# Kernel tuning notes

Hardware: AMD Instinct MI355X
Metric: run time of the kernel (lower is better)

Reference implementation:

```python
import jax, jax.numpy as jnp
import numpy as np

B, P, N, E = 32, 1024, 1024, 128
HQ = 128  # head_num * qkv_dim == embedding_dim
SQRT_E = 11.313708498984761
LOGIT_CLIP = 10.0


def setup_inputs() -> dict:
    key = jax.random.key(0)
    ks = jax.random.split(key, 16)
    s = 1.0 / np.sqrt(E)
    return {
        "encoded_nodes": jax.random.normal(ks[0], (B, N, E), jnp.float32),
        "encoded_q1": jax.random.normal(ks[1], (B, P, E), jnp.float32),
        "encoded_q2": jax.random.normal(ks[2], (B, P, E), jnp.float32),
        "encoded_last_node": jax.random.normal(ks[3], (B, P, E), jnp.float32),
        "load": jax.random.uniform(ks[4], (B, P), jnp.float32),
        "left": jax.random.uniform(ks[5], (B, P), jnp.float32),
        "cur_dist": jax.random.uniform(ks[6], (B, P, N), jnp.float32),
        "log_scale": jnp.ones((), jnp.float32),
        "ninf_mask": jnp.zeros((B, P, N), jnp.float32),
        "Wq1": jax.random.normal(ks[7], (E, HQ), jnp.float32) * s,
        "Wq2": jax.random.normal(ks[8], (E, HQ), jnp.float32) * s,
        "Wq_last": jax.random.normal(ks[9], (E + 2, HQ), jnp.float32) * s,
        "Wk": jax.random.normal(ks[10], (E, HQ), jnp.float32) * s,
        "Wv": jax.random.normal(ks[11], (E, HQ), jnp.float32) * s,
        "AFT_dist_alpha": jnp.ones((1,), jnp.float32),
        "probs_dist_alpha": jnp.ones((1,), jnp.float32),
    }


def reference(encoded_nodes, encoded_q1, encoded_q2, encoded_last_node, load, left,
              cur_dist, log_scale, ninf_mask, Wq1, Wq2, Wq_last, Wk, Wv,
              AFT_dist_alpha, probs_dist_alpha):
    # set_kv / set_q1 / set_q2
    k = encoded_nodes @ Wk                      # [B,N,HQ]
    v = encoded_nodes @ Wv                      # [B,N,HQ]
    single_head_key = jnp.swapaxes(encoded_nodes, 1, 2)  # [B,E,N]
    q1 = encoded_q1 @ Wq1                       # [B,P,HQ]
    q2 = encoded_q2 @ Wq2

    input_cat = jnp.concatenate([encoded_last_node, load[:, :, None], left[:, :, None]], axis=2)
    q_last = input_cat @ Wq_last                # [B,P,HQ]
    q = q1 + q2 + q_last

    cur_dist_out = -cur_dist                    # [B,P,N]
    sigmoid_q = jax.nn.sigmoid(q)
    bias_scale = log_scale * AFT_dist_alpha[0] * cur_dist_out + ninf_mask
    e_bias = jnp.exp(bias_scale)                # [B,P,N]
    ek = jnp.exp(k)                             # [B,N,HQ]
    num = jnp.nan_to_num(jnp.einsum('bpn,bnd->bpd', e_bias, ek * v))
    den = jnp.nan_to_num(jnp.einsum('bpn,bnd->bpd', e_bias, ek)) + 1e-20
    AFT_out = sigmoid_q * (num / den)           # [B,P,HQ]

    score = jnp.einsum('bpd,bdn->bpn', AFT_out, single_head_key)
    score_scaled = score / SQRT_E + log_scale * probs_dist_alpha[0] * cur_dist_out
    score_clipped = LOGIT_CLIP * jnp.tanh(score_scaled)
    probs = jax.nn.softmax(score_clipped + ninf_mask, axis=2)
    return probs
```

## Files before the change

### kernel.cpp

```cpp
#include <hip/hip_runtime.h>
#include <math.h>

#define Bb 32
#define Pp 1024
#define Nn 1024

typedef unsigned short u16;
typedef __bf16 bf16x8 __attribute__((ext_vector_type(8)));
typedef float f32x4 __attribute__((ext_vector_type(4)));
typedef u16 us8 __attribute__((ext_vector_type(8)));
typedef u16 us4 __attribute__((ext_vector_type(4)));

#define MFMA __builtin_amdgcn_mfma_f32_16x16x32_bf16

static constexpr float INV_SQRT_E = 0.08838834764831845f;

__device__ __forceinline__ bf16x8 asbf(us8 v) { return __builtin_bit_cast(bf16x8, v); }

__device__ __forceinline__ void bsplit(float x, u16& h, u16& l) {
  unsigned u = __float_as_uint(x);
  unsigned r = u + 0x7FFF + ((u >> 16) & 1);
  h = (u16)(r >> 16);
  float hf = __uint_as_float((unsigned)h << 16);
  float lof = x - hf;
  unsigned u2 = __float_as_uint(lof);
  unsigned r2 = u2 + 0x7FFF + ((u2 >> 16) & 1);
  l = (u16)(r2 >> 16);
}

__device__ __forceinline__ void tsplit(float x, u16& h, u16& l) {
  unsigned u = __float_as_uint(x);
  h = (u16)(u >> 16);
  float lof = x - __uint_as_float(u & 0xFFFF0000u);
  l = (u16)(__float_as_uint(lof) >> 16);
}

__device__ __forceinline__ float exp10tanh(float s) {
  float ax = fabsf(s);
  float u = __expf(-2.0f * ax);
  float r = __builtin_amdgcn_rcpf(1.0f + u);
  float tt = fmaf(-2.0f * u, r, 1.0f);
  tt = copysignf(tt, s);
  return __expf(10.0f * tt);
}

__global__ __launch_bounds__(256) void prep_weights(
    const float* __restrict__ Wq1, const float* __restrict__ Wq2,
    const float* __restrict__ Wql, const float* __restrict__ Wk,
    const float* __restrict__ Wv, u16* __restrict__ wcat_hi, u16* __restrict__ wcat_lo,
    u16* __restrict__ wkv_hi, u16* __restrict__ wkv_lo) {
  int t = threadIdx.x;
  if (blockIdx.x == 0) {
    for (int i = t; i < 128 * 384; i += 256) {
      int c = i / 384, k = i % 384;
      float v = (k < 128) ? Wq1[k * 128 + c]
                          : (k < 256) ? Wq2[(k - 128) * 128 + c] : Wql[(k - 256) * 128 + c];
      u16 h, l;
      bsplit(v, h, l);
      wcat_hi[i] = h;
      wcat_lo[i] = l;
    }
  } else {
    for (int i = t; i < 256 * 128; i += 256) {
      int c = i >> 7, k = i & 127;
      float v = (c < 128) ? Wk[k * 128 + c] : Wv[k * 128 + (c - 128)];
      u16 h, l;
      bsplit(v, h, l);
      wkv_hi[i] = h;
      wkv_lo[i] = l;
    }
  }
}

__global__ __launch_bounds__(256, 1) void kv_prep(
    const float* __restrict__ nodes, const u16* __restrict__ wkv_hi,
    const u16* __restrict__ wkv_lo, u16* __restrict__ ekkP_hi, u16* __restrict__ ekkP_lo,
    u16* __restrict__ nodesP_hi, u16* __restrict__ nodesP_lo) {
  __shared__ u16 a_hi[32 * 136], a_lo[32 * 136];
  __shared__ float kvbuf[32 * 264];
  const int t = threadIdx.x;
  const int xcd = blockIdx.x & 7, jj = blockIdx.x >> 3;
  const int b = xcd * 4 + (jj >> 5);
  const int n0 = (jj & 31) * 32;
  for (int i = t; i < 4096; i += 256) {
    int n = i >> 7, d = i & 127;
    float v = nodes[((long)(b * 1024 + n0 + n)) * 128 + d];
    u16 h, l;
    bsplit(v, h, l);
    a_hi[n * 136 + d] = h;
    a_lo[n * 136 + d] = l;
  }
  __syncthreads();
  const int lane = t & 63, w = t >> 6;
  const int lr = lane & 15, lg = lane >> 4;
  f32x4 acc0[2][4] = {}, acc1[2][4] = {};
#pragma unroll
  for (int ks = 0; ks < 4; ++ks) {
    us8 ah[2], al[2];
#pragma unroll
    for (int mt = 0; mt < 2; ++mt) {
      int ro = (lr + 16 * mt) * 136 + ks * 32 + lg * 8;
      ah[mt] = *(const us8*)&a_hi[ro];
      al[mt] = *(const us8*)&a_lo[ro];
    }
    us8 bh[4], bl[4];
#pragma unroll
    for (int cc = 0; cc < 4; ++cc) {
      long off = (long)((w * 4 + cc) * 16 + lr) * 128 + ks * 32 + lg * 8;
      bh[cc] = *(const us8*)&wkv_hi[off];
      bl[cc] = *(const us8*)&wkv_lo[off];
    }
#pragma unroll
    for (int mt = 0; mt < 2; ++mt)
#pragma unroll
      for (int cc = 0; cc < 4; ++cc) {
        acc0[mt][cc] = MFMA(asbf(ah[mt]), asbf(bh[cc]), acc0[mt][cc], 0, 0, 0);
        acc1[mt][cc] = MFMA(asbf(al[mt]), asbf(bh[cc]), acc1[mt][cc], 0, 0, 0);
        acc1[mt][cc] = MFMA(asbf(ah[mt]), asbf(bl[cc]), acc1[mt][cc], 0, 0, 0);
      }
  }
#pragma unroll
  for (int mt = 0; mt < 2; ++mt)
#pragma unroll
    for (int cc = 0; cc < 4; ++cc) {
      int c = (w * 4 + cc) * 16 + lr;
#pragma unroll
      for (int r = 0; r < 4; ++r)
        kvbuf[(lg * 4 + r + 16 * mt) * 264 + c] = acc0[mt][cc][r] + acc1[mt][cc][r];
    }
  __syncthreads();
#pragma unroll
  for (int jo = 0; jo < 4; ++jo) {
    int c = jo * 64 + (t & 63);
    int i4 = t >> 6;
    int kcol = (c < 128) ? c : (c - 128);
    us8 h8, l8;
#pragma unroll
    for (int jq = 0; jq < 8; ++jq) {
      int n = i4 * 8 + jq;
      float kv = kvbuf[n * 264 + kcol];
      float ek = __expf(kv);
      float val = (c < 128) ? ek * kvbuf[n * 264 + c + 128] : ek;
      u16 h, l;
      bsplit(val, h, l);
      h8[jq] = h;
      l8[jq] = l;
    }
    long o = (((long)b * 128 + (n0 >> 3) + i4) * 256 + c) * 8;
    *(us8*)&ekkP_hi[o] = h8;
    *(us8*)&ekkP_lo[o] = l8;
  }
  {
    int pl = t >> 7, r = t & 127;
    int dgrp = r >> 3, nb = r & 7;
    const u16* src = pl ? a_lo : a_hi;
    u16* dst = pl ? nodesP_lo : nodesP_hi;
#pragma unroll
    for (int i = 0; i < 4; ++i) {
      int n = nb + 8 * i;
      us8 v = *(const us8*)&src[n * 136 + dgrp * 8];
      *(us8*)&dst[(((long)(b * 16 + dgrp)) * 1024 + n0 + n) * 8] = v;
    }
  }
}

__global__ __launch_bounds__(256) void qsig_prep(
    const float* __restrict__ q1m, const float* __restrict__ q2m,
    const float* __restrict__ lnm, const float* __restrict__ loadv,
    const float* __restrict__ leftv, const float* __restrict__ Wql,
    const u16* __restrict__ wcat_hi, const u16* __restrict__ wcat_lo,
    float* __restrict__ qsig) {
  const int t = threadIdx.x;
  const int lane = t & 63, w = t >> 6;
  const int lr = lane & 15, lg = lane >> 4;
  const long p0 = (long)blockIdx.x * 16;
  const long arow = p0 + lr;
  f32x4 qacc[2] = {};
#pragma unroll 2
  for (int s = 0; s < 12; ++s) {
    const float* __restrict__ src = (s < 4) ? q1m : (s < 8) ? q2m : lnm;
    long ao = arow * 128 + (s & 3) * 32 + lg * 8;
    float4 a0 = *(const float4*)&src[ao];
    float4 a1 = *(const float4*)&src[ao + 4];
    float av[8] = {a0.x, a0.y, a0.z, a0.w, a1.x, a1.y, a1.z, a1.w};
    us8 ah, al;
#pragma unroll
    for (int jq = 0; jq < 8; ++jq) {
      u16 hh, ll;
      tsplit(av[jq], hh, ll);
      ah[jq] = hh;
      al[jq] = ll;
    }
#pragma unroll
    for (int cf = 0; cf < 2; ++cf) {
      int c = w * 32 + cf * 16 + lr;
      us8 bh = *(const us8*)&wcat_hi[c * 384 + s * 32 + lg * 8];
      us8 bl = *(const us8*)&wcat_lo[c * 384 + s * 32 + lg * 8];
      qacc[cf] = MFMA(asbf(ah), asbf(bh), qacc[cf], 0, 0, 0);
      qacc[cf] = MFMA(asbf(al), asbf(bh), qacc[cf], 0, 0, 0);
      qacc[cf] = MFMA(asbf(ah), asbf(bl), qacc[cf], 0, 0, 0);
    }
  }
#pragma unroll
  for (int cf = 0; cf < 2; ++cf) {
    int c = w * 32 + cf * 16 + lr;
    float wl1 = Wql[128 * 128 + c], wl2 = Wql[129 * 128 + c];
#pragma unroll
    for (int r = 0; r < 4; ++r) {
      int row = lg * 4 + r;
      float qv = qacc[cf][r] + loadv[p0 + row] * wl1 + leftv[p0 + row] * wl2;
      qsig[(p0 + row) * 128 + c] = 1.0f / (1.0f + __expf(-qv));
    }
  }
}

__global__ __launch_bounds__(256, 3) void ndaft_gemm(
    const float* __restrict__ cdist, const float* __restrict__ ninf,
    const u16* __restrict__ ekkP_hi, const u16* __restrict__ ekkP_lo,
    const float* __restrict__ qsig, u16* __restrict__ aftP_hi,
    u16* __restrict__ aftP_lo, u16* __restrict__ bias16,
    const float* __restrict__ logs, const float* __restrict__ aal,
    const float* __restrict__ pal) {
  __shared__ u16 lds[18432];
  const int t = threadIdx.x;
  const int lane = t & 63, w = t >> 6;
  const int lr = lane & 15, lg = lane >> 4;
  const int wr = w >> 1, wc = w & 1;
  const int xcd = blockIdx.x & 7, g = blockIdx.x >> 3;
  const int b = xcd * 4 + (g & 3);
  const int pt = g >> 2;
  const long bp = (long)b * Pp + pt * 32;
  const float c1 = logs[0] * aal[0];
  const float c2 = logs[0] * pal[0];

  const int srow = (t < 128) ? (t >> 2) : 0;
  const int soct = t & 3;
  const long arow = bp + srow;
  const long tbase = (arow >> 4) * 32768;
  const int pr = srow & 15, ptile = srow >> 4;

  float4 d0, d1, f0, f1;
  us8 bst[8];
  auto load_regs = [&](int s) {
    if (t < 128) {
      long ao = arow * 1024 + s * 32 + soct * 8;
      d0 = *(const float4*)&cdist[ao];
      d1 = *(const float4*)&cdist[ao + 4];
      f0 = *(const float4*)&ninf[ao];
      f1 = *(const float4*)&ninf[ao + 4];
    }
#pragma unroll
    for (int i = 0; i < 8; ++i) {
      int u = i * 256 + t;
      int oct = u >> 9, pl = (u >> 8) & 1, c = u & 255;
      const u16* bP = pl ? ekkP_lo : ekkP_hi;
      bst[i] = *(const us8*)&bP[(((long)b * 128 + s * 4 + oct) * 256 + c) * 8];
    }
  };

  us8 ebh, ebl;
  auto compute_eb = [&](int s) {
    if (t >= 128) return;
    float dv[8] = {d0.x, d0.y, d0.z, d0.w, d1.x, d1.y, d1.z, d1.w};
    float nv[8] = {f0.x, f0.y, f0.z, f0.w, f1.x, f1.y, f1.z, f1.w};
    us8 q8;
#pragma unroll
    for (int jq = 0; jq < 8; ++jq) {
      float e = __expf(fmaf(-c1, dv[jq], nv[jq]));
      u16 h, l;
      tsplit(e, h, l);
      ebh[jq] = h;
      ebl[jq] = l;
      float x = fminf(fmaxf(c2 * dv[jq], 0.f), 15.999f);
      q8[jq] = (nv[jq] < -1e5f) ? (u16)0xFFFF : (u16)(x * 4096.f + 0.5f);
    }
    *(us8*)&bias16[tbase + ((s * 4 + soct) * 16 + pr) * 8] = q8;
  };

  auto write_lds = [&]() {
    if (t < 128) {
      *(us8*)&lds[((ptile * 2 + 0) * 4 + soct) * 128 + pr * 8] = ebh;
      *(us8*)&lds[((ptile * 2 + 1) * 4 + soct) * 128 + pr * 8] = ebl;
    }
#pragma unroll
    for (int i = 0; i < 8; ++i) {
      int u = i * 256 + t;
      int oct = u >> 9, pl = (u >> 8) & 1, c = u & 255;
      *(us8*)&lds[2048 + ((oct * 2 + pl) * 256 + c) * 8] = bst[i];
    }
  };

  f32x4 acc[8] = {};
  load_regs(0);
  for (int s = 0; s < 32; ++s) {
    compute_eb(s);
    __syncthreads();
    write_lds();
    __syncthreads();
    if (s < 31) load_regs(s + 1);
    us8 ah = *(const us8*)&lds[((wr * 2 + 0) * 4 + lg) * 128 + lr * 8];
    us8 al = *(const us8*)&lds[((wr * 2 + 1) * 4 + lg) * 128 + lr * 8];
#pragma unroll
    for (int ct = 0; ct < 8; ++ct) {
      int c = (ct < 4) ? (wc * 64 + ct * 16 + lr) : (128 + wc * 64 + (ct - 4) * 16 + lr);
      us8 bh = *(const us8*)&lds[2048 + ((lg * 2 + 0) * 256 + c) * 8];
      us8 bl = *(const us8*)&lds[2048 + ((lg * 2 + 1) * 256 + c) * 8];
      acc[ct] = MFMA(asbf(ah), asbf(bh), acc[ct], 0, 0, 0);
      acc[ct] = MFMA(asbf(al), asbf(bh), acc[ct], 0, 0, 0);
      acc[ct] = MFMA(asbf(ah), asbf(bl), acc[ct], 0, 0, 0);
    }
  }
#pragma unroll
  for (int ct = 0; ct < 4; ++ct) {
    int cn = wc * 64 + ct * 16 + lr;
    int nc = cn >> 3, jq = cn & 7;
#pragma unroll
    for (int r = 0; r < 4; ++r) {
      long gr = bp + wr * 16 + lg * 4 + r;
      float sig = qsig[gr * 128 + cn];
      float aftv = sig * acc[ct][r] * __builtin_amdgcn_rcpf(acc[ct + 4][r] + 1e-20f);
      u16 h, l;
      bsplit(aftv, h, l);
      long idx = (gr >> 4) * 2048 + (nc * 16 + (gr & 15)) * 8 + jq;
      aftP_hi[idx] = h;
      aftP_lo[idx] = l;
    }
  }
}

__global__ __launch_bounds__(256, 4) void score_softmax(
    const u16* bias16, const u16* __restrict__ aftP_hi, const u16* __restrict__ aftP_lo,
    const u16* __restrict__ nodesP_hi, const u16* __restrict__ nodesP_lo,
    float* out) {
  __shared__ float psum[16 * 4];
  __shared__ float invb[16];
  const int t = threadIdx.x;
  const int lane = t & 63, w = t >> 6;
  const int lr = lane & 15, lg = lane >> 4;
  const int xcd = blockIdx.x & 7, j = blockIdx.x >> 3;
  const int b = xcd * 4 + (j >> 6);
  const int tl = j & 63;
  const int p0 = tl * 16;
  const long bp = (long)b * Pp + p0;
  const int tile = b * 64 + tl;

  f32x4 sacc[16] = {};
#pragma unroll
  for (int ks = 0; ks < 4; ++ks) {
    long aoff = (long)tile * 2048 + ((long)((ks * 4 + lg) * 16 + lr)) * 8;
    us8 ah = *(const us8*)&aftP_hi[aoff];
    us8 al = *(const us8*)&aftP_lo[aoff];
    long nb = ((long)(b * 16 + ks * 4 + lg)) * 1024;
    auto bld = [&](int cf, us8& bh, us8& bl) {
      long o = (nb + w * 256 + cf * 16 + lr) * 8;
      bh = *(const us8*)&nodesP_hi[o];
      bl = *(const us8*)&nodesP_lo[o];
    };
    us8 bh0, bl0, bh1, bl1;
    bld(0, bh0, bl0);
    bld(1, bh1, bl1);
#pragma unroll
    for (int cf = 0; cf < 16; ++cf) {
      us8 nh = bh1, nl = bl1;
      if (cf < 14) bld(cf + 2, nh, nl);
      sacc[cf] = MFMA(asbf(bh0), asbf(ah), sacc[cf], 0, 0, 0);
      sacc[cf] = MFMA(asbf(bl0), asbf(ah), sacc[cf], 0, 0, 0);
      sacc[cf] = MFMA(asbf(bh0), asbf(al), sacc[cf], 0, 0, 0);
      bh0 = bh1; bl0 = bl1; bh1 = nh; bl1 = nl;
    }
  }

  const long btile = (long)tile * 32768;
  float rs = 0.f;
#pragma unroll
  for (int cf = 0; cf < 16; ++cf) {
    int nc = w * 32 + cf * 2 + (lg >> 1);
    int j0 = (lg & 1) * 4;
    us4 q4 = *(const us4*)&bias16[btile + (nc * 16 + lr) * 8 + j0];
#pragma unroll
    for (int r = 0; r < 4; ++r) {
      u16 qv = q4[r];
      float sv = fmaf(sacc[cf][r], INV_SQRT_E, (float)qv * -2.44140625e-4f);
      float e = exp10tanh(sv);
      e = (qv == (u16)0xFFFF) ? 0.f : e;
      sacc[cf][r] = e;
      rs += e;
    }
  }
  rs += __shfl_xor(rs, 16);
  rs += __shfl_xor(rs, 32);
  if (lane < 16) psum[lr * 4 + w] = rs;
  __syncthreads();
  if (t < 16)
    invb[t] = 1.0f / (psum[t * 4] + psum[t * 4 + 1] + psum[t * 4 + 2] + psum[t * 4 + 3]);
  __syncthreads();

  const float inv = invb[lr];
  const long ro = (bp + lr) * (long)Nn + w * 256;
#pragma unroll
  for (int cf = 0; cf < 16; ++cf) {
    float4 v;
    v.x = sacc[cf][0] * inv;
    v.y = sacc[cf][1] * inv;
    v.z = sacc[cf][2] * inv;
    v.w = sacc[cf][3] * inv;
    *(float4*)&out[ro + cf * 16 + lg * 4] = v;
  }
}

extern "C" void kernel_launch(void* const* d_in, const int* in_sizes, int n_in,
                              void* d_out, int out_size, void* d_ws, size_t ws_size,
                              hipStream_t stream) {
  const float* nodes = (const float*)d_in[0];
  const float* q1m = (const float*)d_in[1];
  const float* q2m = (const float*)d_in[2];
  const float* lnm = (const float*)d_in[3];
  const float* loadv = (const float*)d_in[4];
  const float* leftv = (const float*)d_in[5];
  const float* cdist = (const float*)d_in[6];
  const float* logs = (const float*)d_in[7];
  const float* ninf = (const float*)d_in[8];
  const float* Wq1 = (const float*)d_in[9];
  const float* Wq2 = (const float*)d_in[10];
  const float* Wql = (const float*)d_in[11];
  const float* Wk = (const float*)d_in[12];
  const float* Wv = (const float*)d_in[13];
  const float* aalpha = (const float*)d_in[14];
  const float* palpha = (const float*)d_in[15];

  char* ws = (char*)d_ws;
  u16* ekkP_hi = (u16*)ws;
  u16* ekkP_lo = (u16*)(ws + (16ul << 20));
  u16* nodesP_hi = (u16*)(ws + (32ul << 20));
  u16* nodesP_lo = (u16*)(ws + (40ul << 20));
  float* qsig = (float*)(ws + (48ul << 20));
  u16* aftP_hi = (u16*)(ws + (64ul << 20));
  u16* aftP_lo = (u16*)(ws + (72ul << 20));
  u16* wcat_hi = (u16*)(ws + (80ul << 20));
  u16* wcat_lo = wcat_hi + 128 * 384;
  u16* wkv_hi = wcat_lo + 128 * 384;
  u16* wkv_lo = wkv_hi + 256 * 128;
  u16* bias16 = (u16*)d_out;

  prep_weights<<<2, 256, 0, stream>>>(Wq1, Wq2, Wql, Wk, Wv, wcat_hi, wcat_lo, wkv_hi, wkv_lo);
  kv_prep<<<Bb * Nn / 32, 256, 0, stream>>>(nodes, wkv_hi, wkv_lo, ekkP_hi, ekkP_lo,
                                            nodesP_hi, nodesP_lo);
  qsig_prep<<<2048, 256, 0, stream>>>(q1m, q2m, lnm, loadv, leftv, Wql, wcat_hi, wcat_lo,
                                      qsig);
  ndaft_gemm<<<1024, 256, 0, stream>>>(cdist, ninf, ekkP_hi, ekkP_lo, qsig, aftP_hi,
                                       aftP_lo, bias16, logs, aalpha, palpha);
  score_softmax<<<Bb * Pp / 16, 256, 0, stream>>>(
      bias16, aftP_hi, aftP_lo, nodesP_hi, nodesP_lo, (float*)d_out);
}
```

Before: 373.0 us.

## Enlarge ndaft_gemm tile to 128 rows per block with 512 threads

The AFT GEMM block now covers 128 query rows instead of 32 and uses 8 waves in a 2x4 layout, each holding 4x4 accumulator tiles. Each staged chunk of exp(k)*v and exp(k) is therefore reused across four times as many rows, which cuts redundant global loads of the B operand. All threads now take part in computing the exp bias, and the A-side LDS stride is padded to 136 to reduce bank conflicts. The grid shrinks to 256 blocks, so there are fewer blocks per CU and more register pressure.

```diff
diff --git a/kernel.cpp b/kernel.cpp
--- a/kernel.cpp
+++ b/kernel.cpp
@@ -214,53 +214,49 @@
   }
 }
 
-__global__ __launch_bounds__(256, 3) void ndaft_gemm(
+__global__ __launch_bounds__(512, 2) void ndaft_gemm(
     const float* __restrict__ cdist, const float* __restrict__ ninf,
     const u16* __restrict__ ekkP_hi, const u16* __restrict__ ekkP_lo,
     const float* __restrict__ qsig, u16* __restrict__ aftP_hi,
     u16* __restrict__ aftP_lo, u16* __restrict__ bias16,
     const float* __restrict__ logs, const float* __restrict__ aal,
     const float* __restrict__ pal) {
-  __shared__ u16 lds[18432];
+  __shared__ u16 lds[25088];
   const int t = threadIdx.x;
   const int lane = t & 63, w = t >> 6;
   const int lr = lane & 15, lg = lane >> 4;
-  const int wr = w >> 1, wc = w & 1;
-  const int xcd = blockIdx.x & 7, g = blockIdx.x >> 3;
-  const int b = xcd * 4 + (g & 3);
-  const int pt = g >> 2;
-  const long bp = (long)b * Pp + pt * 32;
+  const int wr = w >> 2, wc = w & 3;
+  const int xcd = blockIdx.x & 7, j = blockIdx.x >> 3;
+  const int b = xcd * 4 + (j & 3);
+  const int pt = j >> 2;
+  const long bp = (long)b * Pp + pt * 128;
   const float c1 = logs[0] * aal[0];
   const float c2 = logs[0] * pal[0];
 
-  const int srow = (t < 128) ? (t >> 2) : 0;
-  const int soct = t & 3;
+  const int srow = t >> 2, soct = t & 3;
   const long arow = bp + srow;
   const long tbase = (arow >> 4) * 32768;
-  const int pr = srow & 15, ptile = srow >> 4;
+  const int spr = srow & 15, sptile = srow >> 4;
+  const long bsrc = (long)b * 128 * 2048;
 
   float4 d0, d1, f0, f1;
-  us8 bst[8];
+  us8 bst[4];
   auto load_regs = [&](int s) {
-    if (t < 128) {
-      long ao = arow * 1024 + s * 32 + soct * 8;
-      d0 = *(const float4*)&cdist[ao];
-      d1 = *(const float4*)&cdist[ao + 4];
-      f0 = *(const float4*)&ninf[ao];
-      f1 = *(const float4*)&ninf[ao + 4];
-    }
-#pragma unroll
-    for (int i = 0; i < 8; ++i) {
-      int u = i * 256 + t;
-      int oct = u >> 9, pl = (u >> 8) & 1, c = u & 255;
-      const u16* bP = pl ? ekkP_lo : ekkP_hi;
-      bst[i] = *(const us8*)&bP[(((long)b * 128 + s * 4 + oct) * 256 + c) * 8];
+    long ao = arow * 1024 + s * 32 + soct * 8;
+    d0 = *(const float4*)&cdist[ao];
+    d1 = *(const float4*)&cdist[ao + 4];
+    f0 = *(const float4*)&ninf[ao];
+    f1 = *(const float4*)&ninf[ao + 4];
+    long sb = bsrc + (long)s * 8192;
+#pragma unroll
+    for (int i = 0; i < 2; ++i) {
+      bst[i] = *(const us8*)&ekkP_hi[sb + (i * 512 + t) * 8];
+      bst[i + 2] = *(const us8*)&ekkP_lo[sb + (i * 512 + t) * 8];
     }
   };
 
   us8 ebh, ebl;
   auto compute_eb = [&](int s) {
-    if (t >= 128) return;
     float dv[8] = {d0.x, d0.y, d0.z, d0.w, d1.x, d1.y, d1.z, d1.w};
     float nv[8] = {f0.x, f0.y, f0.z, f0.w, f1.x, f1.y, f1.z, f1.w};
     us8 q8;
@@ -274,23 +270,20 @@
       float x = fminf(fmaxf(c2 * dv[jq], 0.f), 15.999f);
       q8[jq] = (nv[jq] < -1e5f) ? (u16)0xFFFF : (u16)(x * 4096.f + 0.5f);
     }
-    *(us8*)&bias16[tbase + ((s * 4 + soct) * 16 + pr) * 8] = q8;
+    *(us8*)&bias16[tbase + ((s * 4 + soct) * 16 + spr) * 8] = q8;
   };
 
   auto write_lds = [&]() {
-    if (t < 128) {
-      *(us8*)&lds[((ptile * 2 + 0) * 4 + soct) * 128 + pr * 8] = ebh;
-      *(us8*)&lds[((ptile * 2 + 1) * 4 + soct) * 128 + pr * 8] = ebl;
-    }
-#pragma unroll
-    for (int i = 0; i < 8; ++i) {
-      int u = i * 256 + t;
-      int oct = u >> 9, pl = (u >> 8) & 1, c = u & 255;
-      *(us8*)&lds[2048 + ((oct * 2 + pl) * 256 + c) * 8] = bst[i];
+    *(us8*)&lds[((sptile * 2 + 0) * 4 + soct) * 136 + spr * 8] = ebh;
+    *(us8*)&lds[((sptile * 2 + 1) * 4 + soct) * 136 + spr * 8] = ebl;
+#pragma unroll
+    for (int i = 0; i < 2; ++i) {
+      *(us8*)&lds[8704 + (i * 512 + t) * 8] = bst[i];
+      *(us8*)&lds[8704 + 8192 + (i * 512 + t) * 8] = bst[i + 2];
     }
   };
 
-  f32x4 acc[8] = {};
+  f32x4 acc[4][4] = {};
   load_regs(0);
   for (int s = 0; s < 32; ++s) {
     compute_eb(s);
@@ -298,34 +291,44 @@
     write_lds();
     __syncthreads();
     if (s < 31) load_regs(s + 1);
-    us8 ah = *(const us8*)&lds[((wr * 2 + 0) * 4 + lg) * 128 + lr * 8];
-    us8 al = *(const us8*)&lds[((wr * 2 + 1) * 4 + lg) * 128 + lr * 8];
-#pragma unroll
-    for (int ct = 0; ct < 8; ++ct) {
-      int c = (ct < 4) ? (wc * 64 + ct * 16 + lr) : (128 + wc * 64 + (ct - 4) * 16 + lr);
-      us8 bh = *(const us8*)&lds[2048 + ((lg * 2 + 0) * 256 + c) * 8];
-      us8 bl = *(const us8*)&lds[2048 + ((lg * 2 + 1) * 256 + c) * 8];
-      acc[ct] = MFMA(asbf(ah), asbf(bh), acc[ct], 0, 0, 0);
-      acc[ct] = MFMA(asbf(al), asbf(bh), acc[ct], 0, 0, 0);
-      acc[ct] = MFMA(asbf(ah), asbf(bl), acc[ct], 0, 0, 0);
-    }
-  }
-#pragma unroll
-  for (int ct = 0; ct < 4; ++ct) {
-    int cn = wc * 64 + ct * 16 + lr;
-    int nc = cn >> 3, jq = cn & 7;
-#pragma unroll
-    for (int r = 0; r < 4; ++r) {
-      long gr = bp + wr * 16 + lg * 4 + r;
-      float sig = qsig[gr * 128 + cn];
-      float aftv = sig * acc[ct][r] * __builtin_amdgcn_rcpf(acc[ct + 4][r] + 1e-20f);
-      u16 h, l;
-      bsplit(aftv, h, l);
-      long idx = (gr >> 4) * 2048 + (nc * 16 + (gr & 15)) * 8 + jq;
-      aftP_hi[idx] = h;
-      aftP_lo[idx] = l;
-    }
-  }
+    us8 ah[4], al[4];
+#pragma unroll
+    for (int mt = 0; mt < 4; ++mt) {
+      int ptl = wr * 4 + mt;
+      ah[mt] = *(const us8*)&lds[((ptl * 2 + 0) * 4 + lg) * 136 + lr * 8];
+      al[mt] = *(const us8*)&lds[((ptl * 2 + 1) * 4 + lg) * 136 + lr * 8];
+    }
+#pragma unroll
+    for (int ct = 0; ct < 4; ++ct) {
+      int c = (ct < 2) ? (wc * 32 + ct * 16 + lr) : (96 + wc * 32 + ct * 16 + lr);
+      us8 bh = *(const us8*)&lds[8704 + lg * 2048 + c * 8];
+      us8 bl = *(const us8*)&lds[8704 + 8192 + lg * 2048 + c * 8];
+#pragma unroll
+      for (int mt = 0; mt < 4; ++mt) {
+        acc[mt][ct] = MFMA(asbf(ah[mt]), asbf(bh), acc[mt][ct], 0, 0, 0);
+        acc[mt][ct] = MFMA(asbf(al[mt]), asbf(bh), acc[mt][ct], 0, 0, 0);
+        acc[mt][ct] = MFMA(asbf(ah[mt]), asbf(bl), acc[mt][ct], 0, 0, 0);
+      }
+    }
+  }
+#pragma unroll
+  for (int mt = 0; mt < 4; ++mt)
+#pragma unroll
+    for (int ct = 0; ct < 2; ++ct) {
+      int cn = wc * 32 + ct * 16 + lr;
+      int nc = cn >> 3, jq = cn & 7;
+#pragma unroll
+      for (int r = 0; r < 4; ++r) {
+        long gr = bp + wr * 64 + mt * 16 + lg * 4 + r;
+        float sig = qsig[gr * 128 + cn];
+        float aftv = sig * acc[mt][ct][r] * __builtin_amdgcn_rcpf(acc[mt][ct + 2][r] + 1e-20f);
+        u16 h, l;
+        bsplit(aftv, h, l);
+        long idx = (gr >> 4) * 2048 + (nc * 16 + (gr & 15)) * 8 + jq;
+        aftP_hi[idx] = h;
+        aftP_lo[idx] = l;
+      }
+    }
 }
 
 __global__ __launch_bounds__(256, 4) void score_softmax(
@@ -447,8 +450,8 @@
                                             nodesP_hi, nodesP_lo);
   qsig_prep<<<2048, 256, 0, stream>>>(q1m, q2m, lnm, loadv, leftv, Wql, wcat_hi, wcat_lo,
                                       qsig);
-  ndaft_gemm<<<1024, 256, 0, stream>>>(cdist, ninf, ekkP_hi, ekkP_lo, qsig, aftP_hi,
-                                       aftP_lo, bias16, logs, aalpha, palpha);
+  ndaft_gemm<<<256, 512, 0, stream>>>(cdist, ninf, ekkP_hi, ekkP_lo, qsig, aftP_hi,
+                                      aftP_lo, bias16, logs, aalpha, palpha);
   score_softmax<<<Bb * Pp / 16, 256, 0, stream>>>(
       bias16, aftP_hi, aftP_lo, nodesP_hi, nodesP_lo, (float*)d_out);
 }
```

Result: faster. 363.5 us (-2.5%).
